# Kernel tuning notes

Measured on AMD Instinct MI355X. Metric: run time of the kernel, lower is better.

## Reference

```python
import jax, jax.numpy as jnp
import numpy as np

N_GRIDS = 16
N_FEATS = 2
GRID_SHAPE = (64, 64, 64)  # D, H, W
NODES = 64
N_OUT = 1
DATA_MIN = 0.0
DATA_MAX = 1.0
N_POINTS = 524288


def setup_inputs() -> dict:
    key = jax.random.key(0)
    ks = jax.random.split(key, 12)
    x = jax.random.uniform(ks[0], (N_POINTS, 3), jnp.float32, -1.0, 1.0)
    # matches randomize_grids(): scales ~ log(1 - U*0.05), rotations ~ identity quat + noise,
    # translations ~ U(-0.05, 0.05)
    scales = jnp.log(1.0 - jax.random.uniform(ks[1], (N_GRIDS, 3), jnp.float32) * 0.05)
    rotations = jnp.zeros((N_GRIDS, 4), jnp.float32).at[:, 3].set(1.0) \
        + jax.random.normal(ks[2], (N_GRIDS, 4), jnp.float32) * 0.05
    translations = jax.random.uniform(ks[3], (N_GRIDS, 3), jnp.float32) * 0.1 - 0.05
    # original uses U(-1e-4, 1e-4); use a larger scale for numerically meaningful outputs
    feature_grids = jax.random.uniform(ks[4], (N_GRIDS, N_FEATS) + GRID_SHAPE,
                                       jnp.float32, -0.1, 0.1)
    d_in = N_GRIDS * N_FEATS
    def xavier(k, fi, fo):
        std = np.sqrt(2.0 / (fi + fo)).astype(np.float32)
        return jax.random.normal(k, (fi, fo), jnp.float32) * std
    W0 = xavier(ks[5], d_in, NODES)
    b0 = jax.random.normal(ks[6], (NODES,), jnp.float32) * 0.001
    W1 = xavier(ks[7], NODES, NODES)
    b1 = jax.random.normal(ks[8], (NODES,), jnp.float32) * 0.001
    W2 = xavier(ks[9], NODES, N_OUT)
    b2 = jax.random.normal(ks[10], (N_OUT,), jnp.float32) * 0.001
    return {"x": x, "rotations": rotations, "scales": scales,
            "translations": translations, "feature_grids": feature_grids,
            "W0": W0, "b0": b0, "W1": W1, "b1": b1, "W2": W2, "b2": b2}


def quat_to_rot(q):
    # q: [G,4] in (x, y, z, w) order; normalized (rotation_activation)
    q = q / jnp.linalg.norm(q, axis=-1, keepdims=True)
    x, y, z, w = q[:, 0], q[:, 1], q[:, 2], q[:, 3]
    r0 = jnp.stack([1 - 2 * (y * y + z * z), 2 * (x * y - z * w), 2 * (x * z + y * w)], -1)
    r1 = jnp.stack([2 * (x * y + z * w), 1 - 2 * (x * x + z * z), 2 * (y * z - x * w)], -1)
    r2 = jnp.stack([2 * (x * z - y * w), 2 * (y * z + x * w), 1 - 2 * (x * x + y * y)], -1)
    return jnp.stack([r0, r1, r2], axis=-2)  # [G,3,3]


def transform_points(x, rotations, scales, translations):
    # S*R*T order: local = diag(exp(scales)) @ R @ x + t, per grid -> [G,N,3]
    R = quat_to_rot(rotations)
    s = jnp.exp(scales)
    M = s[:, :, None] * R  # [G,3,3]
    return jnp.einsum('gij,nj->gni', M, x) + translations[:, None, :]


def trilinear_sample(grid, pts):
    # grid: [C,D,H,W]; pts: [N,3] (x,y,z) in [-1,1]; grid_sample semantics:
    # mode='bilinear', align_corners=True, padding_mode='zeros'
    C, D, H, W = grid.shape
    fx = (pts[:, 0] + 1.0) * 0.5 * (W - 1)
    fy = (pts[:, 1] + 1.0) * 0.5 * (H - 1)
    fz = (pts[:, 2] + 1.0) * 0.5 * (D - 1)
    x0 = jnp.floor(fx); y0 = jnp.floor(fy); z0 = jnp.floor(fz)
    wx = fx - x0; wy = fy - y0; wz = fz - z0
    x0i = x0.astype(jnp.int32); y0i = y0.astype(jnp.int32); z0i = z0.astype(jnp.int32)

    def corner(dx, dy, dz):
        xi = x0i + dx; yi = y0i + dy; zi = z0i + dz
        valid = (xi >= 0) & (xi < W) & (yi >= 0) & (yi < H) & (zi >= 0) & (zi < D)
        v = grid[:, jnp.clip(zi, 0, D - 1), jnp.clip(yi, 0, H - 1), jnp.clip(xi, 0, W - 1)]
        w = ((wx if dx else 1 - wx) * (wy if dy else 1 - wy) * (wz if dz else 1 - wz))
        return v * jnp.where(valid, w, 0.0)[None, :]

    out = corner(0, 0, 0)
    for dz in (0, 1):
        for dy in (0, 1):
            for dx in (0, 1):
                if (dx, dy, dz) != (0, 0, 0):
                    out = out + corner(dx, dy, dz)
    return out  # [C,N]


def reference(x, rotations, scales, translations, feature_grids, W0, b0, W1, b1, W2, b2):
    pts = transform_points(x, rotations, scales, translations)      # [G,N,3]
    feats = jax.vmap(trilinear_sample)(feature_grids, pts)          # [G,C,N]
    feats = feats.transpose(2, 0, 1).reshape(x.shape[0], -1)        # [N, G*C]
    h = jax.nn.relu(feats @ W0 + b0)
    h = jax.nn.relu(h @ W1 + b1)
    y = h @ W2 + b2
    return y * (DATA_MAX - DATA_MIN) + DATA_MIN
```

## Files before the change

kernel.cpp:

```cpp
#include <hip/hip_runtime.h>
#include <cstddef>
#include <cstdint>

constexpr int NPTS   = 524288;
constexpr int NG     = 16;
constexpr int GR     = 64;
constexpr int GR3    = GR * GR * GR;
constexpr int NNODES = 64;
constexpr int NBINS  = 32768;

constexpr size_t GRIDS_BYTES = (size_t)NG * GR3 * 8;
constexpr size_t WS_SORT     = GRIDS_BYTES;
constexpr size_t SORT_BYTES  = (size_t)NPTS * 16;
constexpr size_t WS_KEYR     = WS_SORT + SORT_BYTES;
constexpr size_t KEYR_BYTES  = (size_t)NPTS * 4;
constexpr size_t WS_BINS     = WS_KEYR + KEYR_BYTES;
constexpr size_t BINS_BYTES  = (size_t)NBINS * 4;
constexpr size_t WS_MATS     = WS_BINS + BINS_BYTES;
constexpr size_t MATS_BYTES  = 1024;
constexpr size_t WS_WPACK    = WS_MATS + MATS_BYTES;
constexpr size_t WPACK_BYTES = (size_t)(256 + 512) * 16;
constexpr size_t WS_PART     = WS_WPACK + WPACK_BYTES;
constexpr size_t PART_BYTES  = 128 * 4;
constexpr size_t WS_TOTAL    = WS_PART + PART_BYTES;

constexpr int PREP_REPACK = 4096;
constexpr int PREP_HIST   = 2048;

typedef _Float16 half8 __attribute__((ext_vector_type(8)));
typedef float    floatx4 __attribute__((ext_vector_type(4)));

__device__ __forceinline__ unsigned part1by2(unsigned x) {
    x &= 0x3ff;
    x = (x | (x << 16)) & 0x030000FF;
    x = (x | (x <<  8)) & 0x0300F00F;
    x = (x | (x <<  4)) & 0x030C30C3;
    x = (x | (x <<  2)) & 0x09249249;
    return x;
}

__device__ __forceinline__ unsigned cell_of(float px, float py, float pz) {
    int cx = (int)((px + 1.0f) * 16.0f); cx = min(max(cx, 0), 31);
    int cy = (int)((py + 1.0f) * 16.0f); cy = min(max(cy, 0), 31);
    int cz = (int)((pz + 1.0f) * 16.0f); cz = min(max(cz, 0), 31);
    return part1by2((unsigned)cx) | (part1by2((unsigned)cy) << 1) | (part1by2((unsigned)cz) << 2);
}

__device__ __forceinline__ unsigned f32_to_bf16_rne(float f) {
    unsigned u = __float_as_uint(f);
    return (u + 0x7fffu + ((u >> 16) & 1u)) >> 16;
}

__device__ __forceinline__ unsigned pack_h2(float a, float b) {
    unsigned short ua = __builtin_bit_cast(unsigned short, (_Float16)a);
    unsigned short ub = __builtin_bit_cast(unsigned short, (_Float16)b);
    return (unsigned)ua | ((unsigned)ub << 16);
}

__device__ __forceinline__ unsigned short f32_to_h16(float a) {
    return __builtin_bit_cast(unsigned short, (_Float16)a);
}

__global__ __launch_bounds__(256) void prep_kernel(
    const float* __restrict__ grids, uint2* __restrict__ gout,
    const float* __restrict__ xs, unsigned* __restrict__ bins,
    unsigned* __restrict__ keyrank,
    const float* __restrict__ rot, const float* __restrict__ scl,
    const float* __restrict__ trn, float* __restrict__ mats,
    const float* __restrict__ W0, const float* __restrict__ W1,
    uint4* __restrict__ wpack)
{
    const int bid = blockIdx.x;
    const int tid = threadIdx.x;

    if (bid < PREP_REPACK) {
        const int base = (bid * 256 + tid) * 4;
        const int g    = base >> 18;
        const int node = base & (GR3 - 1);
        const int x    = node & 63;
        const float* p0 = grids + (size_t)g * 2 * GR3 + node;
        const float* p1 = p0 + GR3;
        const float4 c0 = *(const float4*)p0;
        const float4 c1 = *(const float4*)p1;
        float d0n, d1n;
        if (x == 60) { d0n = c0.w; d1n = c1.w; }
        else         { d0n = p0[4]; d1n = p1[4]; }
        const float e0[5] = {c0.x, c0.y, c0.z, c0.w, d0n};
        const float e1[5] = {c1.x, c1.y, c1.z, c1.w, d1n};
        unsigned pk[5];
        #pragma unroll
        for (int i = 0; i < 5; ++i)
            pk[i] = f32_to_bf16_rne(e0[i]) | (f32_to_bf16_rne(e1[i]) << 16);
        uint4* dst = (uint4*)(gout + (size_t)g * GR3 + node);
        dst[0] = make_uint4(pk[0], pk[1], pk[1], pk[2]);
        dst[1] = make_uint4(pk[2], pk[3], pk[3], pk[4]);
    } else if (bid < PREP_REPACK + PREP_HIST) {
        const int n = (bid - PREP_REPACK) * 256 + tid;
        const unsigned key = cell_of(xs[n*3+0], xs[n*3+1], xs[n*3+2]);
        const unsigned rank = atomicAdd(&bins[key], 1u);
        keyrank[n] = key | (rank << 15);
    } else if (bid == PREP_REPACK + PREP_HIST) {
        const int g = tid;
        if (g < NG) {
            float qx = rot[g*4+0], qy = rot[g*4+1], qz = rot[g*4+2], qw = rot[g*4+3];
            const float inv = 1.0f / sqrtf(qx*qx + qy*qy + qz*qz + qw*qw);
            qx *= inv; qy *= inv; qz *= inv; qw *= inv;
            const float sx = expf(scl[g*3+0]);
            const float sy = expf(scl[g*3+1]);
            const float sz = expf(scl[g*3+2]);
            float* m = mats + g * 12;
            m[0] = sx * (1.0f - 2.0f*(qy*qy + qz*qz));
            m[1] = sx * (2.0f*(qx*qy - qz*qw));
            m[2] = sx * (2.0f*(qx*qz + qy*qw));
            m[3] = sy * (2.0f*(qx*qy + qz*qw));
            m[4] = sy * (1.0f - 2.0f*(qx*qx + qz*qz));
            m[5] = sy * (2.0f*(qy*qz - qx*qw));
            m[6] = sz * (2.0f*(qx*qz - qy*qw));
            m[7] = sz * (2.0f*(qy*qz + qx*qw));
            m[8] = sz * (1.0f - 2.0f*(qx*qx + qy*qy));
            m[9]  = trn[g*3+0];
            m[10] = trn[g*3+1];
            m[11] = trn[g*3+2];
        }
    } else {
        const int t = tid >> 6;
        const int lane = tid & 63;
        const int q = lane >> 4, c = lane & 15;
        const int n = t * 16 + c;
        {
            unsigned u[4];
            #pragma unroll
            for (int jj = 0; jj < 4; ++jj) {
                const int k0 = q * 8 + 2 * jj;
                u[jj] = pack_h2(W0[k0 * NNODES + n], W0[(k0 + 1) * NNODES + n]);
            }
            wpack[t * 64 + lane] = make_uint4(u[0], u[1], u[2], u[3]);
        }
        #pragma unroll
        for (int ks = 0; ks < 2; ++ks) {
            unsigned u[4];
            #pragma unroll
            for (int jj = 0; jj < 4; ++jj) {
                const int k0 = ks * 32 + q * 8 + 2 * jj;
                u[jj] = pack_h2(W1[k0 * NNODES + n], W1[(k0 + 1) * NNODES + n]);
            }
            wpack[256 + (ks * 4 + t) * 64 + lane] = make_uint4(u[0], u[1], u[2], u[3]);
        }
    }
}

__global__ __launch_bounds__(256) void scanA_kernel(unsigned* __restrict__ bins,
                                                    unsigned* __restrict__ part) {
    __shared__ unsigned s[256];
    const int t = threadIdx.x;
    const int base = blockIdx.x * 256;
    const unsigned v = bins[base + t];
    s[t] = v;
    __syncthreads();
    for (int off = 1; off < 256; off <<= 1) {
        unsigned u = (t >= off) ? s[t - off] : 0u;
        __syncthreads();
        s[t] += u;
        __syncthreads();
    }
    bins[base + t] = s[t] - v;
    if (t == 255) part[blockIdx.x] = s[255];
}

__global__ __launch_bounds__(128) void scanB_kernel(unsigned* __restrict__ part) {
    __shared__ unsigned s[128];
    const int t = threadIdx.x;
    const unsigned v = part[t];
    s[t] = v;
    __syncthreads();
    for (int off = 1; off < 128; off <<= 1) {
        unsigned u = (t >= off) ? s[t - off] : 0u;
        __syncthreads();
        s[t] += u;
        __syncthreads();
    }
    part[t] = s[t] - v;
}

__global__ __launch_bounds__(256) void scatter_kernel(const float* __restrict__ xs,
                                                      const unsigned* __restrict__ bins,
                                                      const unsigned* __restrict__ part,
                                                      const unsigned* __restrict__ keyrank,
                                                      float4* __restrict__ sorted) {
    const int n = blockIdx.x * 256 + threadIdx.x;
    if (n >= NPTS) return;
    const unsigned kr = keyrank[n];
    const unsigned key = kr & 0x7fffu;
    const unsigned rank = kr >> 15;
    const unsigned pos = part[key >> 8] + bins[key] + rank;
    sorted[pos] = make_float4(xs[n*3+0], xs[n*3+1], xs[n*3+2], __int_as_float(n));
}

struct Geom {
    int i00, i01, i10, i11;
    float ax0, ax1, ay0, ay1, az0, az1;
    unsigned selhi, sello;
};

__device__ __forceinline__ Geom make_geom(const float* __restrict__ m,
                                          float px, float py, float pz, int g) {
    Geom G;
    const float tx = fmaf(m[0], px, fmaf(m[1], py, fmaf(m[2], pz, m[9])));
    const float ty = fmaf(m[3], px, fmaf(m[4], py, fmaf(m[5], pz, m[10])));
    const float tz = fmaf(m[6], px, fmaf(m[7], py, fmaf(m[8], pz, m[11])));
    const float fx = (tx + 1.0f) * 31.5f;
    const float fy = (ty + 1.0f) * 31.5f;
    const float fz = (tz + 1.0f) * 31.5f;
    const float x0f = floorf(fx), y0f = floorf(fy), z0f = floorf(fz);
    const float wx = fx - x0f, wy = fy - y0f, wz = fz - z0f;
    const int x0 = (int)x0f, y0 = (int)y0f, z0 = (int)z0f;
    G.ax0 = ((unsigned)x0       < 64u) ? (1.0f - wx) : 0.0f;
    G.ax1 = ((unsigned)(x0 + 1) < 64u) ? wx          : 0.0f;
    G.ay0 = ((unsigned)y0       < 64u) ? (1.0f - wy) : 0.0f;
    G.ay1 = ((unsigned)(y0 + 1) < 64u) ? wy          : 0.0f;
    G.az0 = ((unsigned)z0       < 64u) ? (1.0f - wz) : 0.0f;
    G.az1 = ((unsigned)(z0 + 1) < 64u) ? wz          : 0.0f;
    G.selhi = (x0 >= 63) ? 1u : 0u;
    G.sello = (x0 <= -1) ? 1u : 0u;
    const int xb  = min(max(x0, 0), 62);
    const int yc0 = min(max(y0, 0), 63),     yc1 = min(max(y0 + 1, 0), 63);
    const int zc0 = min(max(z0, 0), 63),     zc1 = min(max(z0 + 1, 0), 63);
    const int b = (g << 18) + xb;
    G.i00 = b + (zc0 << 12) + (yc0 << 6);
    G.i01 = b + (zc0 << 12) + (yc1 << 6);
    G.i10 = b + (zc1 << 12) + (yc0 << 6);
    G.i11 = b + (zc1 << 12) + (yc1 << 6);
    return G;
}

__device__ __forceinline__ void acc_pair(float& f0, float& f1, const Geom& G,
                                         uint2 q, float wyz) {
    const unsigned v0 = G.selhi ? q.y : q.x;
    const unsigned v1 = G.sello ? q.x : q.y;
    float s0 = G.ax0 * __uint_as_float(v0 << 16);
    s0 = fmaf(G.ax1, __uint_as_float(v1 << 16), s0);
    f0 = fmaf(wyz, s0, f0);
    float s1 = G.ax0 * __uint_as_float(v0 & 0xffff0000u);
    s1 = fmaf(G.ax1, __uint_as_float(v1 & 0xffff0000u), s1);
    f1 = fmaf(wyz, s1, f1);
}

constexpr int HSTR    = 72;
constexpr int ARENA_H = 64 * HSTR;
constexpr int FSTRIDE = 40;

__global__ __launch_bounds__(256, 4) void amgsrn_main(
    const float4* __restrict__ sorted,
    const uint2*  __restrict__ gridsP,
    const float*  __restrict__ mats,
    const uint4*  __restrict__ wpack,
    const float*  __restrict__ b0,
    const float*  __restrict__ b1,
    const float*  __restrict__ W2,
    const float*  __restrict__ b2,
    float* __restrict__ out)
{
    __shared__ unsigned short sh[4 * ARENA_H];
    __shared__ float yS[256];

    const int tid  = threadIdx.x;
    const int lane = tid & 63;
    const int wv   = tid >> 6;
    const int c    = lane & 15;
    const int q    = lane >> 4;
    unsigned short* wa = sh + wv * ARENA_H;

    const int n = blockIdx.x * 256 + tid;
    const float4 p = sorted[n];
    const float px = p.x, py = p.y, pz = p.z;
    const int orig = __float_as_int(p.w);

    unsigned pk[NG];
    Geom Ga = make_geom(mats, px, py, pz, 0);
    uint2 a00 = gridsP[Ga.i00], a01 = gridsP[Ga.i01];
    uint2 a10 = gridsP[Ga.i10], a11 = gridsP[Ga.i11];
    Geom Gb = make_geom(mats + 12, px, py, pz, 1);
    uint2 b00 = gridsP[Gb.i00], b01 = gridsP[Gb.i01];
    uint2 b10 = gridsP[Gb.i10], b11 = gridsP[Gb.i11];
    #pragma unroll
    for (int g = 0; g < NG; ++g) {
        Geom Gn;
        uint2 n00, n01, n10, n11;
        if (g + 2 < NG) {
            Gn = make_geom(mats + (g + 2) * 12, px, py, pz, g + 2);
            n00 = gridsP[Gn.i00]; n01 = gridsP[Gn.i01];
            n10 = gridsP[Gn.i10]; n11 = gridsP[Gn.i11];
        }
        float f0 = 0.0f, f1 = 0.0f;
        acc_pair(f0, f1, Ga, a00, Ga.az0 * Ga.ay0);
        acc_pair(f0, f1, Ga, a01, Ga.az0 * Ga.ay1);
        acc_pair(f0, f1, Ga, a10, Ga.az1 * Ga.ay0);
        acc_pair(f0, f1, Ga, a11, Ga.az1 * Ga.ay1);
        pk[g] = pack_h2(f0, f1);
        Ga = Gb; a00 = b00; a01 = b01; a10 = b10; a11 = b11;
        if (g + 2 < NG) {
            Gb = Gn; b00 = n00; b01 = n01; b10 = n10; b11 = n11;
        }
    }

    {
        uint4* dst = (uint4*)(wa + lane * FSTRIDE);
        dst[0] = make_uint4(pk[0],  pk[1],  pk[2],  pk[3]);
        dst[1] = make_uint4(pk[4],  pk[5],  pk[6],  pk[7]);
        dst[2] = make_uint4(pk[8],  pk[9],  pk[10], pk[11]);
        dst[3] = make_uint4(pk[12], pk[13], pk[14], pk[15]);
    }
    __syncthreads();

    half8 a0[4];
    #pragma unroll
    for (int m = 0; m < 4; ++m)
        a0[m] = *(const half8*)(wa + (m * 16 + c) * FSTRIDE + q * 8);

    half8 b0f[4], b1f[2][4];
    #pragma unroll
    for (int t = 0; t < 4; ++t)
        b0f[t] = __builtin_bit_cast(half8, wpack[t * 64 + lane]);
    #pragma unroll
    for (int ks = 0; ks < 2; ++ks)
        #pragma unroll
        for (int t = 0; t < 4; ++t)
            b1f[ks][t] = __builtin_bit_cast(half8, wpack[256 + (ks * 4 + t) * 64 + lane]);
    float b0v[4], b1v[4], w2v[4];
    #pragma unroll
    for (int t = 0; t < 4; ++t) {
        b0v[t] = b0[t * 16 + c];
        b1v[t] = b1[t * 16 + c];
        w2v[t] = W2[t * 16 + c];
    }
    const float b2s = b2[0];

    __syncthreads();

    #pragma unroll
    for (int t = 0; t < 4; ++t) {
        #pragma unroll
        for (int m = 0; m < 4; ++m) {
            floatx4 acc = {b0v[t], b0v[t], b0v[t], b0v[t]};
            acc = __builtin_amdgcn_mfma_f32_16x16x32_f16(a0[m], b0f[t], acc, 0, 0, 0);
            const int node = t * 16 + c;
            const int ptb  = m * 16 + q * 4;
            #pragma unroll
            for (int r = 0; r < 4; ++r)
                wa[(ptb + r) * HSTR + node] = f32_to_h16(fmaxf(acc[r], 0.0f));
        }
    }
    __syncthreads();

    half8 a1[4][2];
    #pragma unroll
    for (int m = 0; m < 4; ++m)
        #pragma unroll
        for (int ks = 0; ks < 2; ++ks)
            a1[m][ks] = *(const half8*)(wa + (m * 16 + c) * HSTR + ks * 32 + q * 8);

    float p4[4][4];
    #pragma unroll
    for (int m = 0; m < 4; ++m)
        #pragma unroll
        for (int r = 0; r < 4; ++r) p4[m][r] = 0.0f;

    #pragma unroll
    for (int t = 0; t < 4; ++t) {
        #pragma unroll
        for (int m = 0; m < 4; ++m) {
            floatx4 acc = {b1v[t], b1v[t], b1v[t], b1v[t]};
            acc = __builtin_amdgcn_mfma_f32_16x16x32_f16(a1[m][0], b1f[0][t], acc, 0, 0, 0);
            acc = __builtin_amdgcn_mfma_f32_16x16x32_f16(a1[m][1], b1f[1][t], acc, 0, 0, 0);
            #pragma unroll
            for (int r = 0; r < 4; ++r)
                p4[m][r] = fmaf(fmaxf(acc[r], 0.0f), w2v[t], p4[m][r]);
        }
    }

    #pragma unroll
    for (int m = 0; m < 4; ++m)
        #pragma unroll
        for (int r = 0; r < 4; ++r) {
            float v = p4[m][r];
            v += __shfl_xor(v, 1, 64);
            v += __shfl_xor(v, 2, 64);
            v += __shfl_xor(v, 4, 64);
            v += __shfl_xor(v, 8, 64);
            p4[m][r] = v + b2s;
        }

    if (c == 0) {
        #pragma unroll
        for (int m = 0; m < 4; ++m)
            #pragma unroll
            for (int r = 0; r < 4; ++r)
                yS[wv * 64 + m * 16 + q * 4 + r] = p4[m][r];
    }
    __syncthreads();
    out[orig] = yS[tid];
}

__global__ __launch_bounds__(256, 3) void amgsrn_fused_fallback(
    const float* __restrict__ xs,
    const float* __restrict__ rot,
    const float* __restrict__ scl,
    const float* __restrict__ trn,
    const float* __restrict__ grids,
    const float* __restrict__ W0,
    const float* __restrict__ b0,
    const float* __restrict__ W1,
    const float* __restrict__ b1,
    const float* __restrict__ W2,
    const float* __restrict__ b2,
    float* __restrict__ out)
{
    __shared__ float sM[NG][12];
    const int tid = threadIdx.x;
    if (tid < NG) {
        const int g = tid;
        float qx = rot[g*4+0], qy = rot[g*4+1], qz = rot[g*4+2], qw = rot[g*4+3];
        const float inv = 1.0f / sqrtf(qx*qx + qy*qy + qz*qz + qw*qw);
        qx *= inv; qy *= inv; qz *= inv; qw *= inv;
        const float sx = expf(scl[g*3+0]);
        const float sy = expf(scl[g*3+1]);
        const float sz = expf(scl[g*3+2]);
        sM[g][0] = sx * (1.0f - 2.0f*(qy*qy + qz*qz));
        sM[g][1] = sx * (2.0f*(qx*qy - qz*qw));
        sM[g][2] = sx * (2.0f*(qx*qz + qy*qw));
        sM[g][3] = sy * (2.0f*(qx*qy + qz*qw));
        sM[g][4] = sy * (1.0f - 2.0f*(qx*qx + qz*qz));
        sM[g][5] = sy * (2.0f*(qy*qz - qx*qw));
        sM[g][6] = sz * (2.0f*(qx*qz - qy*qw));
        sM[g][7] = sz * (2.0f*(qy*qz + qx*qw));
        sM[g][8] = sz * (1.0f - 2.0f*(qx*qx + qy*qy));
        sM[g][9]  = trn[g*3+0];
        sM[g][10] = trn[g*3+1];
        sM[g][11] = trn[g*3+2];
    }
    __syncthreads();

    const int n = blockIdx.x * blockDim.x + tid;
    if (n >= NPTS) return;
    const float px = xs[n*3+0];
    const float py = xs[n*3+1];
    const float pz = xs[n*3+2];

    float h0[NNODES];
    #pragma unroll
    for (int j = 0; j < NNODES; ++j) h0[j] = b0[j];

    #pragma unroll
    for (int g = 0; g < NG; ++g) {
        const float* m = sM[g];
        const float tx = m[0]*px + m[1]*py + m[2]*pz + m[9];
        const float ty = m[3]*px + m[4]*py + m[5]*pz + m[10];
        const float tz = m[6]*px + m[7]*py + m[8]*pz + m[11];
        const float fx = (tx + 1.0f) * 31.5f;
        const float fy = (ty + 1.0f) * 31.5f;
        const float fz = (tz + 1.0f) * 31.5f;
        const float x0f = floorf(fx), y0f = floorf(fy), z0f = floorf(fz);
        const float wx = fx - x0f, wy = fy - y0f, wz = fz - z0f;
        const int x0 = (int)x0f, y0 = (int)y0f, z0 = (int)z0f;
        const float* gb = grids + (size_t)g * (size_t)(2 * GR3);
        float f0 = 0.0f, f1 = 0.0f;
        #pragma unroll
        for (int dz = 0; dz < 2; ++dz) {
            #pragma unroll
            for (int dy = 0; dy < 2; ++dy) {
                #pragma unroll
                for (int dx = 0; dx < 2; ++dx) {
                    const int xi = x0 + dx, yi = y0 + dy, zi = z0 + dz;
                    const bool valid = ((unsigned)xi < (unsigned)GR) &
                                       ((unsigned)yi < (unsigned)GR) &
                                       ((unsigned)zi < (unsigned)GR);
                    const int xc = min(max(xi, 0), GR-1);
                    const int yc = min(max(yi, 0), GR-1);
                    const int zc = min(max(zi, 0), GR-1);
                    float w = (dx ? wx : 1.0f - wx) *
                              (dy ? wy : 1.0f - wy) *
                              (dz ? wz : 1.0f - wz);
                    w = valid ? w : 0.0f;
                    const int idx = (zc * GR + yc) * GR + xc;
                    f0 = fmaf(w, gb[idx], f0);
                    f1 = fmaf(w, gb[idx + GR3], f1);
                }
            }
        }
        const float* w0a = W0 + (2*g    ) * NNODES;
        const float* w0b = W0 + (2*g + 1) * NNODES;
        #pragma unroll
        for (int j = 0; j < NNODES; ++j)
            h0[j] = fmaf(f1, w0b[j], fmaf(f0, w0a[j], h0[j]));
    }
    #pragma unroll
    for (int j = 0; j < NNODES; ++j) h0[j] = fmaxf(h0[j], 0.0f);

    float y = b2[0];
    #pragma unroll
    for (int half = 0; half < 2; ++half) {
        float h1[32];
        #pragma unroll
        for (int j = 0; j < 32; ++j) h1[j] = b1[half * 32 + j];
        #pragma unroll
        for (int k = 0; k < NNODES; ++k) {
            const float a = h0[k];
            const float* w = W1 + k * NNODES + half * 32;
            #pragma unroll
            for (int j = 0; j < 32; ++j) h1[j] = fmaf(a, w[j], h1[j]);
        }
        #pragma unroll
        for (int j = 0; j < 32; ++j) y = fmaf(fmaxf(h1[j], 0.0f), W2[half * 32 + j], y);
    }

    out[n] = y;
}

extern "C" void kernel_launch(void* const* d_in, const int* in_sizes, int n_in,
                              void* d_out, int out_size, void* d_ws, size_t ws_size,
                              hipStream_t stream) {
    const float* xs  = (const float*)d_in[0];
    const float* rot = (const float*)d_in[1];
    const float* scl = (const float*)d_in[2];
    const float* trn = (const float*)d_in[3];
    const float* gr  = (const float*)d_in[4];
    const float* W0  = (const float*)d_in[5];
    const float* b0  = (const float*)d_in[6];
    const float* W1  = (const float*)d_in[7];
    const float* b1  = (const float*)d_in[8];
    const float* W2  = (const float*)d_in[9];
    const float* b2  = (const float*)d_in[10];
    float* out = (float*)d_out;

    if (ws_size < WS_TOTAL) {
        dim3 grid((NPTS + 255) / 256), block(256);
        hipLaunchKernelGGL(amgsrn_fused_fallback, grid, block, 0, stream,
                           xs, rot, scl, trn, gr, W0, b0, W1, b1, W2, b2, out);
        return;
    }

    char* ws = (char*)d_ws;
    uint2*    gridsP  = (uint2*)(ws);
    float4*   sorted  = (float4*)(ws + WS_SORT);
    unsigned* keyrank = (unsigned*)(ws + WS_KEYR);
    unsigned* bins    = (unsigned*)(ws + WS_BINS);
    float*    mats    = (float*)(ws + WS_MATS);
    uint4*    wpack   = (uint4*)(ws + WS_WPACK);
    unsigned* part    = (unsigned*)(ws + WS_PART);

    hipMemsetAsync(bins, 0, BINS_BYTES, stream);
    hipLaunchKernelGGL(prep_kernel, dim3(PREP_REPACK + PREP_HIST + 2), dim3(256), 0, stream,
                       gr, gridsP, xs, bins, keyrank,
                       rot, scl, trn, mats, W0, W1, wpack);
    hipLaunchKernelGGL(scanA_kernel, dim3(NBINS / 256), dim3(256), 0, stream, bins, part);
    hipLaunchKernelGGL(scanB_kernel, dim3(1), dim3(128), 0, stream, part);
    hipLaunchKernelGGL(scatter_kernel, dim3(NPTS / 256), dim3(256), 0, stream,
                       xs, bins, part, keyrank, sorted);
    hipLaunchKernelGGL(amgsrn_main, dim3(NPTS / 256), dim3(256), 0, stream,
                       sorted, gridsP, mats, wpack, b0, b1, W2, b2, out);
}
```

Baseline: 190.5 us.

## Fold scanB into scatter, deepen gather prefetch, swizzle blocks, use wave-level fences

Several independent changes. The repack step reads its neighbor element through a wave shuffle instead of a second global load. The second-level prefix scan now runs inside every scatter block as a wave scan, which removes a kernel launch. The main kernel swizzles block order, keeps grid-corner gathers four grids ahead instead of two, and replaces block barriers with per-wave lgkmcnt waits. The wave-only fences are valid only if each wave touches just its own LDS arena and yS slice, and the deeper prefetch raises register pressure under the launch bound of 4.

```diff
diff --git a/kernel.cpp b/kernel.cpp
--- a/kernel.cpp
+++ b/kernel.cpp
@@ -61,6 +61,10 @@
     return __builtin_bit_cast(unsigned short, (_Float16)a);
 }
 
+__device__ __forceinline__ void wave_fence() {
+    asm volatile("s_waitcnt lgkmcnt(0)" ::: "memory");
+}
+
 __global__ __launch_bounds__(256) void prep_kernel(
     const float* __restrict__ grids, uint2* __restrict__ gout,
     const float* __restrict__ xs, unsigned* __restrict__ bins,
@@ -82,9 +86,12 @@
         const float* p1 = p0 + GR3;
         const float4 c0 = *(const float4*)p0;
         const float4 c1 = *(const float4*)p1;
+        const float s0n = __shfl_down(c0.x, 1, 64);
+        const float s1n = __shfl_down(c1.x, 1, 64);
         float d0n, d1n;
-        if (x == 60) { d0n = c0.w; d1n = c1.w; }
-        else         { d0n = p0[4]; d1n = p1[4]; }
+        if (x == 60)                 { d0n = c0.w;  d1n = c1.w;  }
+        else if ((tid & 63) == 63)   { d0n = p0[4]; d1n = p1[4]; }
+        else                         { d0n = s0n;   d1n = s1n;   }
         const float e0[5] = {c0.x, c0.y, c0.z, c0.w, d0n};
         const float e1[5] = {c1.x, c1.y, c1.z, c1.w, d1n};
         unsigned pk[5];
@@ -167,32 +174,32 @@
     if (t == 255) part[blockIdx.x] = s[255];
 }
 
-__global__ __launch_bounds__(128) void scanB_kernel(unsigned* __restrict__ part) {
-    __shared__ unsigned s[128];
-    const int t = threadIdx.x;
-    const unsigned v = part[t];
-    s[t] = v;
-    __syncthreads();
-    for (int off = 1; off < 128; off <<= 1) {
-        unsigned u = (t >= off) ? s[t - off] : 0u;
-        __syncthreads();
-        s[t] += u;
-        __syncthreads();
-    }
-    part[t] = s[t] - v;
-}
-
 __global__ __launch_bounds__(256) void scatter_kernel(const float* __restrict__ xs,
                                                       const unsigned* __restrict__ bins,
                                                       const unsigned* __restrict__ part,
                                                       const unsigned* __restrict__ keyrank,
                                                       float4* __restrict__ sorted) {
-    const int n = blockIdx.x * 256 + threadIdx.x;
-    if (n >= NPTS) return;
+    __shared__ unsigned sp[128];
+    const int t = threadIdx.x;
+    if (t < 64) {
+        const unsigned a = part[2 * t];
+        const unsigned b = part[2 * t + 1];
+        unsigned s = a + b;
+        #pragma unroll
+        for (int off = 1; off < 64; off <<= 1) {
+            const unsigned u = __shfl_up(s, off, 64);
+            if (t >= off) s += u;
+        }
+        const unsigned excl = s - (a + b);
+        sp[2 * t]     = excl;
+        sp[2 * t + 1] = excl + a;
+    }
+    __syncthreads();
+    const int n = blockIdx.x * 256 + t;
     const unsigned kr = keyrank[n];
     const unsigned key = kr & 0x7fffu;
     const unsigned rank = kr >> 15;
-    const unsigned pos = part[key >> 8] + bins[key] + rank;
+    const unsigned pos = sp[key >> 8] + bins[key] + rank;
     sorted[pos] = make_float4(xs[n*3+0], xs[n*3+1], xs[n*3+2], __int_as_float(n));
 }
 
@@ -248,6 +255,7 @@
 constexpr int HSTR    = 72;
 constexpr int ARENA_H = 64 * HSTR;
 constexpr int FSTRIDE = 40;
+constexpr int MAIN_NB = NPTS / 256;
 
 __global__ __launch_bounds__(256, 4) void amgsrn_main(
     const float4* __restrict__ sorted,
@@ -270,36 +278,35 @@
     const int q    = lane >> 4;
     unsigned short* wa = sh + wv * ARENA_H;
 
-    const int n = blockIdx.x * 256 + tid;
+    const int bid = blockIdx.x;
+    const int swz = (bid & 7) * (MAIN_NB / 8) + (bid >> 3);
+    const int n = swz * 256 + tid;
     const float4 p = sorted[n];
     const float px = p.x, py = p.y, pz = p.z;
     const int orig = __float_as_int(p.w);
 
     unsigned pk[NG];
-    Geom Ga = make_geom(mats, px, py, pz, 0);
-    uint2 a00 = gridsP[Ga.i00], a01 = gridsP[Ga.i01];
-    uint2 a10 = gridsP[Ga.i10], a11 = gridsP[Ga.i11];
-    Geom Gb = make_geom(mats + 12, px, py, pz, 1);
-    uint2 b00 = gridsP[Gb.i00], b01 = gridsP[Gb.i01];
-    uint2 b10 = gridsP[Gb.i10], b11 = gridsP[Gb.i11];
+    Geom Gs[4];
+    uint2 v00[4], v01[4], v10[4], v11[4];
+    #pragma unroll
+    for (int g = 0; g < 4; ++g) {
+        Gs[g] = make_geom(mats + g * 12, px, py, pz, g);
+        v00[g] = gridsP[Gs[g].i00]; v01[g] = gridsP[Gs[g].i01];
+        v10[g] = gridsP[Gs[g].i10]; v11[g] = gridsP[Gs[g].i11];
+    }
     #pragma unroll
     for (int g = 0; g < NG; ++g) {
-        Geom Gn;
-        uint2 n00, n01, n10, n11;
-        if (g + 2 < NG) {
-            Gn = make_geom(mats + (g + 2) * 12, px, py, pz, g + 2);
-            n00 = gridsP[Gn.i00]; n01 = gridsP[Gn.i01];
-            n10 = gridsP[Gn.i10]; n11 = gridsP[Gn.i11];
-        }
+        const int s = g & 3;
         float f0 = 0.0f, f1 = 0.0f;
-        acc_pair(f0, f1, Ga, a00, Ga.az0 * Ga.ay0);
-        acc_pair(f0, f1, Ga, a01, Ga.az0 * Ga.ay1);
-        acc_pair(f0, f1, Ga, a10, Ga.az1 * Ga.ay0);
-        acc_pair(f0, f1, Ga, a11, Ga.az1 * Ga.ay1);
+        acc_pair(f0, f1, Gs[s], v00[s], Gs[s].az0 * Gs[s].ay0);
+        acc_pair(f0, f1, Gs[s], v01[s], Gs[s].az0 * Gs[s].ay1);
+        acc_pair(f0, f1, Gs[s], v10[s], Gs[s].az1 * Gs[s].ay0);
+        acc_pair(f0, f1, Gs[s], v11[s], Gs[s].az1 * Gs[s].ay1);
         pk[g] = pack_h2(f0, f1);
-        Ga = Gb; a00 = b00; a01 = b01; a10 = b10; a11 = b11;
-        if (g + 2 < NG) {
-            Gb = Gn; b00 = n00; b01 = n01; b10 = n10; b11 = n11;
+        if (g + 4 < NG) {
+            Gs[s] = make_geom(mats + (g + 4) * 12, px, py, pz, g + 4);
+            v00[s] = gridsP[Gs[s].i00]; v01[s] = gridsP[Gs[s].i01];
+            v10[s] = gridsP[Gs[s].i10]; v11[s] = gridsP[Gs[s].i11];
         }
     }
 
@@ -310,7 +317,7 @@
         dst[2] = make_uint4(pk[8],  pk[9],  pk[10], pk[11]);
         dst[3] = make_uint4(pk[12], pk[13], pk[14], pk[15]);
     }
-    __syncthreads();
+    wave_fence();
 
     half8 a0[4];
     #pragma unroll
@@ -335,7 +342,7 @@
     }
     const float b2s = b2[0];
 
-    __syncthreads();
+    wave_fence();
 
     #pragma unroll
     for (int t = 0; t < 4; ++t) {
@@ -350,7 +357,7 @@
                 wa[(ptb + r) * HSTR + node] = f32_to_h16(fmaxf(acc[r], 0.0f));
         }
     }
-    __syncthreads();
+    wave_fence();
 
     half8 a1[4][2];
     #pragma unroll
@@ -397,7 +404,7 @@
             for (int r = 0; r < 4; ++r)
                 yS[wv * 64 + m * 16 + q * 4 + r] = p4[m][r];
     }
-    __syncthreads();
+    wave_fence();
     out[orig] = yS[tid];
 }
 
@@ -553,7 +560,6 @@
                        gr, gridsP, xs, bins, keyrank,
                        rot, scl, trn, mats, W0, W1, wpack);
     hipLaunchKernelGGL(scanA_kernel, dim3(NBINS / 256), dim3(256), 0, stream, bins, part);
-    hipLaunchKernelGGL(scanB_kernel, dim3(1), dim3(128), 0, stream, part);
     hipLaunchKernelGGL(scatter_kernel, dim3(NPTS / 256), dim3(256), 0, stream,
                        xs, bins, part, keyrank, sorted);
     hipLaunchKernelGGL(amgsrn_main, dim3(NPTS / 256), dim3(256), 0, stream,
```

Result: faster. 183.5 us (-3.7%).

## Fold partial scan into scatter, swizzle LDS hidden layout, raise occupancy

Applied to the files above, without the earlier changes.

Removes the single-block scanB launch by having every scatter block redo the 128-entry partial prefix scan with wavefront shuffles. In the main kernel it replaces the padded-stride hidden-activation LDS tile with an XOR-swizzled unpadded layout, reuses that arena for the output staging buffer, raises the occupancy hint from 4 to 5 blocks, and remaps block indices so that consecutive blocks are spread across the sorted point range. The grid repack gets its neighbor value from a lane shuffle instead of a second global load. Together these aim to cut launch overhead, LDS footprint and bank conflicts, at the cost of redundant scan work per block and possibly worse cache locality from the block remapping.

```diff
diff --git a/kernel.cpp b/kernel.cpp
--- a/kernel.cpp
+++ b/kernel.cpp
@@ -82,9 +82,12 @@
         const float* p1 = p0 + GR3;
         const float4 c0 = *(const float4*)p0;
         const float4 c1 = *(const float4*)p1;
+        const float s0n = __shfl_down(c0.x, 1, 64);
+        const float s1n = __shfl_down(c1.x, 1, 64);
         float d0n, d1n;
-        if (x == 60) { d0n = c0.w; d1n = c1.w; }
-        else         { d0n = p0[4]; d1n = p1[4]; }
+        if (x == 60)                 { d0n = c0.w;  d1n = c1.w;  }
+        else if ((tid & 63) == 63)   { d0n = p0[4]; d1n = p1[4]; }
+        else                         { d0n = s0n;   d1n = s1n;   }
         const float e0[5] = {c0.x, c0.y, c0.z, c0.w, d0n};
         const float e1[5] = {c1.x, c1.y, c1.z, c1.w, d1n};
         unsigned pk[5];
@@ -167,32 +170,32 @@
     if (t == 255) part[blockIdx.x] = s[255];
 }
 
-__global__ __launch_bounds__(128) void scanB_kernel(unsigned* __restrict__ part) {
-    __shared__ unsigned s[128];
-    const int t = threadIdx.x;
-    const unsigned v = part[t];
-    s[t] = v;
-    __syncthreads();
-    for (int off = 1; off < 128; off <<= 1) {
-        unsigned u = (t >= off) ? s[t - off] : 0u;
-        __syncthreads();
-        s[t] += u;
-        __syncthreads();
-    }
-    part[t] = s[t] - v;
-}
-
 __global__ __launch_bounds__(256) void scatter_kernel(const float* __restrict__ xs,
                                                       const unsigned* __restrict__ bins,
                                                       const unsigned* __restrict__ part,
                                                       const unsigned* __restrict__ keyrank,
                                                       float4* __restrict__ sorted) {
-    const int n = blockIdx.x * 256 + threadIdx.x;
-    if (n >= NPTS) return;
+    __shared__ unsigned sp[128];
+    const int t = threadIdx.x;
+    if (t < 64) {
+        const unsigned a = part[2 * t];
+        const unsigned b = part[2 * t + 1];
+        unsigned s = a + b;
+        #pragma unroll
+        for (int off = 1; off < 64; off <<= 1) {
+            const unsigned u = __shfl_up(s, off, 64);
+            if (t >= off) s += u;
+        }
+        const unsigned excl = s - (a + b);
+        sp[2 * t]     = excl;
+        sp[2 * t + 1] = excl + a;
+    }
+    __syncthreads();
+    const int n = blockIdx.x * 256 + t;
     const unsigned kr = keyrank[n];
     const unsigned key = kr & 0x7fffu;
     const unsigned rank = kr >> 15;
-    const unsigned pos = part[key >> 8] + bins[key] + rank;
+    const unsigned pos = sp[key >> 8] + bins[key] + rank;
     sorted[pos] = make_float4(xs[n*3+0], xs[n*3+1], xs[n*3+2], __int_as_float(n));
 }
 
@@ -245,11 +248,11 @@
     f1 = fmaf(wyz, s1, f1);
 }
 
-constexpr int HSTR    = 72;
-constexpr int ARENA_H = 64 * HSTR;
+constexpr int ARENA_H = 64 * 64;
 constexpr int FSTRIDE = 40;
-
-__global__ __launch_bounds__(256, 4) void amgsrn_main(
+constexpr int MAIN_NB = NPTS / 256;
+
+__global__ __launch_bounds__(256, 5) void amgsrn_main(
     const float4* __restrict__ sorted,
     const uint2*  __restrict__ gridsP,
     const float*  __restrict__ mats,
@@ -261,7 +264,6 @@
     float* __restrict__ out)
 {
     __shared__ unsigned short sh[4 * ARENA_H];
-    __shared__ float yS[256];
 
     const int tid  = threadIdx.x;
     const int lane = tid & 63;
@@ -270,7 +272,9 @@
     const int q    = lane >> 4;
     unsigned short* wa = sh + wv * ARENA_H;
 
-    const int n = blockIdx.x * 256 + tid;
+    const int bid = blockIdx.x;
+    const int swz = (bid & 7) * (MAIN_NB / 8) + (bid >> 3);
+    const int n = swz * 256 + tid;
     const float4 p = sorted[n];
     const float px = p.x, py = p.y, pz = p.z;
     const int orig = __float_as_int(p.w);
@@ -343,21 +347,27 @@
         for (int m = 0; m < 4; ++m) {
             floatx4 acc = {b0v[t], b0v[t], b0v[t], b0v[t]};
             acc = __builtin_amdgcn_mfma_f32_16x16x32_f16(a0[m], b0f[t], acc, 0, 0, 0);
-            const int node = t * 16 + c;
-            const int ptb  = m * 16 + q * 4;
-            #pragma unroll
-            for (int r = 0; r < 4; ++r)
-                wa[(ptb + r) * HSTR + node] = f32_to_h16(fmaxf(acc[r], 0.0f));
+            const int gnode = 2 * t + (c >> 3);
+            const int nlow  = c & 7;
+            const int ptb   = m * 16 + q * 4;
+            #pragma unroll
+            for (int r = 0; r < 4; ++r) {
+                const int row = ptb + r;
+                wa[(row << 6) + ((gnode ^ (row & 7)) << 3) + nlow] =
+                    f32_to_h16(fmaxf(acc[r], 0.0f));
+            }
         }
     }
     __syncthreads();
 
     half8 a1[4][2];
     #pragma unroll
-    for (int m = 0; m < 4; ++m)
+    for (int m = 0; m < 4; ++m) {
+        const int row = m * 16 + c;
         #pragma unroll
         for (int ks = 0; ks < 2; ++ks)
-            a1[m][ks] = *(const half8*)(wa + (m * 16 + c) * HSTR + ks * 32 + q * 8);
+            a1[m][ks] = *(const half8*)(wa + (row << 6) + (((ks * 4 + q) ^ (c & 7)) << 3));
+    }
 
     float p4[4][4];
     #pragma unroll
@@ -390,15 +400,16 @@
             p4[m][r] = v + b2s;
         }
 
+    float* yf = (float*)wa;
     if (c == 0) {
         #pragma unroll
         for (int m = 0; m < 4; ++m)
             #pragma unroll
             for (int r = 0; r < 4; ++r)
-                yS[wv * 64 + m * 16 + q * 4 + r] = p4[m][r];
-    }
-    __syncthreads();
-    out[orig] = yS[tid];
+                yf[m * 16 + q * 4 + r] = p4[m][r];
+    }
+    __syncthreads();
+    out[orig] = yf[lane];
 }
 
 __global__ __launch_bounds__(256, 3) void amgsrn_fused_fallback(
@@ -553,7 +564,6 @@
                        gr, gridsP, xs, bins, keyrank,
                        rot, scl, trn, mats, W0, W1, wpack);
     hipLaunchKernelGGL(scanA_kernel, dim3(NBINS / 256), dim3(256), 0, stream, bins, part);
-    hipLaunchKernelGGL(scanB_kernel, dim3(1), dim3(128), 0, stream, part);
     hipLaunchKernelGGL(scatter_kernel, dim3(NPTS / 256), dim3(256), 0, stream,
                        xs, bins, part, keyrank, sorted);
     hipLaunchKernelGGL(amgsrn_main, dim3(NPTS / 256), dim3(256), 0, stream,
```

Result: slower. 207.2 us (+8.8%).
